# Optimization experiments

Hardware: AMD Instinct MI355X
Metric: run time of the kernel (lower is better)

The kernel has to match this reference:

```python
import jax, jax.numpy as jnp
import numpy as np

H = 128  # hidden size
F_IN = 33  # GRU input size
STEPS = 64


def setup_inputs() -> dict:
    key = jax.random.key(0)
    ks = jax.random.split(key, 10)
    x = jax.random.normal(ks[0], (STEPS, 17), dtype=jnp.float32)
    ip = jax.random.randint(ks[1], (STEPS, 8), 0, 256)
    port = jax.random.randint(ks[2], (STEPS, 2), 0, 70000)
    hidden = jnp.zeros((1, 1, H), dtype=jnp.float32)
    # learned parameters (torch default init ~ U(-1/sqrt(H), 1/sqrt(H)) for GRU, N(0,1) for embeddings)
    s = 1.0 / np.sqrt(H)
    ip_emb = jax.random.normal(ks[3], (256, 1), dtype=jnp.float32)
    port_emb = jax.random.normal(ks[4], (70000, 4), dtype=jnp.float32)
    W_ih = jax.random.uniform(ks[5], (3 * H, F_IN), minval=-s, maxval=s, dtype=jnp.float32)
    W_hh = jax.random.uniform(ks[6], (3 * H, H), minval=-s, maxval=s, dtype=jnp.float32)
    b_ih = jax.random.uniform(ks[7], (3 * H,), minval=-s, maxval=s, dtype=jnp.float32)
    b_hh = jax.random.uniform(ks[8], (3 * H,), minval=-s, maxval=s, dtype=jnp.float32)
    return {"x": x, "ip": ip, "port": port, "hidden": hidden,
            "ip_emb": ip_emb, "port_emb": port_emb,
            "W_ih": W_ih, "W_hh": W_hh, "b_ih": b_ih, "b_hh": b_hh}


def reference(x, ip, port, hidden, ip_emb, port_emb, W_ih, W_hh, b_ih, b_hh):
    # Embedding lookups + flatten: [64, 8*1] and [64, 2*4]
    ipf = ip_emb[ip].reshape(STEPS, -1)
    pf = port_emb[port].reshape(STEPS, -1)
    xi = jnp.concatenate([x, ipf, pf], axis=1)  # [64, 33]
    h0 = hidden[0, 0]  # [128]; same initial hidden reused at every step in the original loop
    # Single batched GRU cell over all 64 "steps" (they are independent given shared h0)
    gi = xi @ W_ih.T + b_ih          # [64, 3H]
    gh = h0 @ W_hh.T + b_hh          # [3H], broadcast over the 64 rows
    i_r, i_z, i_n = jnp.split(gi, 3, axis=1)
    h_r, h_z, h_n = jnp.split(gh, 3)
    r = jax.nn.sigmoid(i_r + h_r)
    z = jax.nn.sigmoid(i_z + h_z)
    n = jnp.tanh(i_n + r * h_n)
    outputs = (1.0 - z) * n + z * h0  # [64, 128]
    new_hidden = outputs[STEPS - 1].reshape(1, 1, H)  # self.hidden after last iteration
    return outputs, new_hidden
```

## Files before the change

### kernel.cpp

```cpp
#include <hip/hip_runtime.h>
#include <hip/hip_bf16.h>

#define H 128
#define STEPS 64
#define F_IN 33
#define R3H 384

__global__ __launch_bounds__(256) void gh_kernel(
    const float* __restrict__ hidden,
    const float* __restrict__ W_hh,
    const float* __restrict__ b_hh,
    float* __restrict__ gh)
{
    const int wave = threadIdx.x >> 6;
    const int lane = threadIdx.x & 63;
    const int row  = blockIdx.x * 4 + wave;
    const float* wrow = W_hh + (size_t)row * H;
    float p = wrow[lane] * hidden[lane] + wrow[lane + 64] * hidden[lane + 64];
    #pragma unroll
    for (int m = 32; m >= 1; m >>= 1) p += __shfl_xor(p, m, 64);
    if (lane == 0) gh[row] = p + b_hh[row];
}

__global__ __launch_bounds__(128) void Encoder_57380763074770_kernel(
    const float* __restrict__ x,
    const int*   __restrict__ ip,
    const int*   __restrict__ port,
    const float* __restrict__ hidden,
    const float* __restrict__ ip_emb,
    const float* __restrict__ port_emb,
    const float* __restrict__ W_ih,
    const float* __restrict__ b_ih,
    const float* __restrict__ gh,
    float* __restrict__ out)
{
    __shared__ float xi[F_IN];
    __shared__ float h0s[H];
    __shared__ float wih[R3H * F_IN];

    const int s   = blockIdx.x;
    const int tid = threadIdx.x;

    if (tid < 17) {
        xi[tid] = x[s * 17 + tid];
    } else if (tid < 25) {
        xi[tid] = ip_emb[ip[s * 8 + (tid - 17)]];
    } else if (tid < F_IN) {
        int c = tid - 25;
        xi[tid] = port_emb[port[s * 2 + (c >> 2)] * 4 + (c & 3)];
    }
    h0s[tid] = hidden[tid];

    {
        const float4* w4 = (const float4*)W_ih;
        float4*       l4 = (float4*)wih;
        #pragma unroll
        for (int i = 0; i < (R3H * F_IN) / 4 / 128 + 1; ++i) {
            int idx = tid + i * 128;
            if (idx < (R3H * F_IN) / 4) l4[idx] = w4[idx];
        }
    }

    const int j = tid;
    const float ghr = gh[j];
    const float ghz = gh[j + H];
    const float ghn = gh[j + 2 * H];
    float gir = b_ih[j];
    float giz = b_ih[j + H];
    float gin = b_ih[j + 2 * H];

    __syncthreads();

    const float* vr = wih + j * F_IN;
    const float* vz = wih + (j + H) * F_IN;
    const float* vn = wih + (j + 2 * H) * F_IN;
    #pragma unroll
    for (int k = 0; k < F_IN; ++k) {
        const float xv = xi[k];
        gir = fmaf(xv, vr[k], gir);
        giz = fmaf(xv, vz[k], giz);
        gin = fmaf(xv, vn[k], gin);
    }

    const float r = 1.0f / (1.0f + __expf(-(gir + ghr)));
    const float z = 1.0f / (1.0f + __expf(-(giz + ghz)));
    float a = gin + r * ghn;
    a = fminf(fmaxf(a, -15.0f), 15.0f);
    const float e2 = __expf(2.0f * a);
    const float n = (e2 - 1.0f) / (e2 + 1.0f);
    const float o = (1.0f - z) * n + z * h0s[j];

    out[s * H + j] = o;
    if (s == STEPS - 1) out[STEPS * H + j] = o;
}

extern "C" void kernel_launch(void* const* d_in, const int* in_sizes, int n_in,
                              void* d_out, int out_size, void* d_ws, size_t ws_size,
                              hipStream_t stream) {
    const float* x        = (const float*)d_in[0];
    const int*   ip       = (const int*)  d_in[1];
    const int*   port     = (const int*)  d_in[2];
    const float* hidden   = (const float*)d_in[3];
    const float* ip_emb   = (const float*)d_in[4];
    const float* port_emb = (const float*)d_in[5];
    const float* W_ih     = (const float*)d_in[6];
    const float* W_hh     = (const float*)d_in[7];
    const float* b_ih     = (const float*)d_in[8];
    const float* b_hh     = (const float*)d_in[9];
    float* out = (float*)d_out;
    float* gh  = (float*)d_ws;

    gh_kernel<<<96, 256, 0, stream>>>(hidden, W_hh, b_hh, gh);
    Encoder_57380763074770_kernel<<<STEPS, H, 0, stream>>>(
        x, ip, port, hidden, ip_emb, port_emb, W_ih, b_ih, gh, out);
}
```

Measured before the change: 77.60 us.

## Fuse hidden-gate matvec into main GRU kernel, removing separate gh launch

Removes the separate gh_kernel launch and the workspace round trip. Each of the 64 blocks now computes the full W_hh·h0 hidden-gate matvec itself, with each thread reading three 128-float rows of W_hh through strided per-thread float4 loads. This saves a kernel launch and a dependency, but it repeats the W_hh work 64 times. The per-thread row access pattern is uncoalesced, which may make the memory load costly.

```diff
diff --git a/kernel.cpp b/kernel.cpp
--- a/kernel.cpp
+++ b/kernel.cpp
@@ -1,26 +1,9 @@
 #include <hip/hip_runtime.h>
-#include <hip/hip_bf16.h>
 
 #define H 128
 #define STEPS 64
 #define F_IN 33
 #define R3H 384
-
-__global__ __launch_bounds__(256) void gh_kernel(
-    const float* __restrict__ hidden,
-    const float* __restrict__ W_hh,
-    const float* __restrict__ b_hh,
-    float* __restrict__ gh)
-{
-    const int wave = threadIdx.x >> 6;
-    const int lane = threadIdx.x & 63;
-    const int row  = blockIdx.x * 4 + wave;
-    const float* wrow = W_hh + (size_t)row * H;
-    float p = wrow[lane] * hidden[lane] + wrow[lane + 64] * hidden[lane + 64];
-    #pragma unroll
-    for (int m = 32; m >= 1; m >>= 1) p += __shfl_xor(p, m, 64);
-    if (lane == 0) gh[row] = p + b_hh[row];
-}
 
 __global__ __launch_bounds__(128) void Encoder_57380763074770_kernel(
     const float* __restrict__ x,
@@ -30,8 +13,9 @@
     const float* __restrict__ ip_emb,
     const float* __restrict__ port_emb,
     const float* __restrict__ W_ih,
+    const float* __restrict__ W_hh,
     const float* __restrict__ b_ih,
-    const float* __restrict__ gh,
+    const float* __restrict__ b_hh,
     float* __restrict__ out)
 {
     __shared__ float xi[F_IN];
@@ -40,6 +24,7 @@
 
     const int s   = blockIdx.x;
     const int tid = threadIdx.x;
+    const int j   = tid;
 
     if (tid < 17) {
         xi[tid] = x[s * 17 + tid];
@@ -55,31 +40,58 @@
         const float4* w4 = (const float4*)W_ih;
         float4*       l4 = (float4*)wih;
         #pragma unroll
-        for (int i = 0; i < (R3H * F_IN) / 4 / 128 + 1; ++i) {
+        for (int i = 0; i < 25; ++i) {
             int idx = tid + i * 128;
             if (idx < (R3H * F_IN) / 4) l4[idx] = w4[idx];
         }
     }
 
-    const int j = tid;
-    const float ghr = gh[j];
-    const float ghz = gh[j + H];
-    const float ghn = gh[j + 2 * H];
+    float ghr = b_hh[j];
+    float ghz = b_hh[j + H];
+    float ghn = b_hh[j + 2 * H];
     float gir = b_ih[j];
     float giz = b_ih[j + H];
     float gin = b_ih[j + 2 * H];
 
     __syncthreads();
 
-    const float* vr = wih + j * F_IN;
-    const float* vz = wih + (j + H) * F_IN;
-    const float* vn = wih + (j + 2 * H) * F_IN;
-    #pragma unroll
-    for (int k = 0; k < F_IN; ++k) {
-        const float xv = xi[k];
-        gir = fmaf(xv, vr[k], gir);
-        giz = fmaf(xv, vz[k], giz);
-        gin = fmaf(xv, vn[k], gin);
+    {
+        const float4* wr = (const float4*)(W_hh + (size_t)j * H);
+        const float4* wz = (const float4*)(W_hh + (size_t)(j + H) * H);
+        const float4* wn = (const float4*)(W_hh + (size_t)(j + 2 * H) * H);
+        const float4* h4 = (const float4*)h0s;
+        #pragma unroll 4
+        for (int k = 0; k < H / 4; ++k) {
+            const float4 hv = h4[k];
+            const float4 ar = wr[k];
+            const float4 az = wz[k];
+            const float4 an = wn[k];
+            ghr = fmaf(hv.x, ar.x, ghr);
+            ghr = fmaf(hv.y, ar.y, ghr);
+            ghr = fmaf(hv.z, ar.z, ghr);
+            ghr = fmaf(hv.w, ar.w, ghr);
+            ghz = fmaf(hv.x, az.x, ghz);
+            ghz = fmaf(hv.y, az.y, ghz);
+            ghz = fmaf(hv.z, az.z, ghz);
+            ghz = fmaf(hv.w, az.w, ghz);
+            ghn = fmaf(hv.x, an.x, ghn);
+            ghn = fmaf(hv.y, an.y, ghn);
+            ghn = fmaf(hv.z, an.z, ghn);
+            ghn = fmaf(hv.w, an.w, ghn);
+        }
+    }
+
+    {
+        const float* vr = wih + j * F_IN;
+        const float* vz = wih + (j + H) * F_IN;
+        const float* vn = wih + (j + 2 * H) * F_IN;
+        #pragma unroll
+        for (int k = 0; k < F_IN; ++k) {
+            const float xv = xi[k];
+            gir = fmaf(xv, vr[k], gir);
+            giz = fmaf(xv, vz[k], giz);
+            gin = fmaf(xv, vn[k], gin);
+        }
     }
 
     const float r = 1.0f / (1.0f + __expf(-(gir + ghr)));
@@ -108,9 +120,8 @@
     const float* b_ih     = (const float*)d_in[8];
     const float* b_hh     = (const float*)d_in[9];
     float* out = (float*)d_out;
-    float* gh  = (float*)d_ws;
+    (void)d_ws; (void)ws_size;
 
-    gh_kernel<<<96, 256, 0, stream>>>(hidden, W_hh, b_hh, gh);
     Encoder_57380763074770_kernel<<<STEPS, H, 0, stream>>>(
-        x, ip, port, hidden, ip_emb, port_emb, W_ih, b_ih, gh, out);
+        x, ip, port, hidden, ip_emb, port_emb, W_ih, W_hh, b_ih, b_hh, out);
 }
```

Measured after the change: 80.27 us. 3.4% more time.
